# Performance work log

Hardware: AMD Instinct MI355X
Metric: run time of the kernel (lower is better)

## Reference

```python
import jax, jax.numpy as jnp
import numpy as np


def setup_inputs() -> dict:
    key = jax.random.key(0)
    k1, k2, k3, k4 = jax.random.split(key, 4)
    c = 256
    x = jax.random.normal(k1, (4, c, 64, 64), dtype=jnp.float32)
    # 1x1 conv weights act as channel-mixing matrices
    w_qkv = jax.random.normal(k2, (3 * c, c), dtype=jnp.float32) * (1.0 / np.sqrt(c))
    w_out = jax.random.normal(k3, (c, c), dtype=jnp.float32) * (1.0 / np.sqrt(c))
    b_out = jax.random.normal(k4, (c,), dtype=jnp.float32) * 0.01
    return {"x": x, "w_qkv": w_qkv, "w_out": w_out, "b_out": b_out}


def reference(x, w_qkv, w_out, b_out):
    b, c, h, w = x.shape
    heads = 4
    d = c // heads
    scale = d ** (-0.5)
    hw = h * w

    # 1x1 conv (no bias): [b,3c,h,w]
    qkv = jnp.einsum('oc,bchw->bohw', w_qkv, x)
    q, k, v = jnp.split(qkv, 3, axis=1)

    def to_seq(t):
        # [b,c,h,w] -> [b,heads,hw,d]
        return t.reshape(b, heads, d, hw).transpose(0, 1, 3, 2)

    q, k, v = to_seq(q), to_seq(k), to_seq(v)

    sim = jnp.einsum('bhid,bhjd->bhij', q, k) * scale
    attn = jax.nn.softmax(sim, axis=-1)
    out = jnp.einsum('bhij,bhjd->bhid', attn, v)

    # [b,heads,hw,d] -> [b,c,h,w]
    out = out.transpose(0, 1, 3, 2).reshape(b, c, h, w)

    # output 1x1 conv with bias, plus residual
    proj = jnp.einsum('oc,bchw->bohw', w_out, out) + b_out[None, :, None, None]
    return x + proj
```

## Files before the change

kernel.cpp:

```cpp
#include <hip/hip_runtime.h>


#define HW 4096
#define CIN 256
#define LOG2E_DIV8 0.18033688011112042f
#define SM_SHIFT 8.0f

typedef __attribute__((ext_vector_type(8))) short short8v;
typedef __attribute__((ext_vector_type(4))) short short4v;
typedef __attribute__((ext_vector_type(4))) float float4v;
typedef __attribute__((ext_vector_type(16))) float f32x16;
typedef __attribute__((ext_vector_type(4))) unsigned int uint4v;

typedef const __attribute__((address_space(1))) unsigned int* gptr_t;
typedef __attribute__((address_space(3))) unsigned int* lptr_t;

static __device__ __forceinline__ unsigned short f2bf(float f) {
    unsigned int u = __float_as_uint(f);
    u += 0x7fff + ((u >> 16) & 1);
    return (unsigned short)(u >> 16);
}
static __device__ __forceinline__ unsigned int pkbf(float a, float b) {
    unsigned int r;
    asm("v_cvt_pk_bf16_f32 %0, %1, %2" : "=v"(r) : "v"(a), "v"(b));
    return r;
}
static __device__ __forceinline__ void pl32swap(unsigned int& a, unsigned int& b) {
    asm volatile("v_permlane32_swap_b32 %0, %1" : "+v"(a), "+v"(b));
}

__global__ __launch_bounds__(256) void cast_all_k(
    const float* __restrict__ w_qkv, const float* __restrict__ w_out,
    const float* __restrict__ x,
    unsigned short* __restrict__ wqb, unsigned short* __restrict__ wob,
    unsigned short* __restrict__ xt)
{
    const int bi = blockIdx.x;
    const int t = threadIdx.x;
    __shared__ float tile[64][65];

    if (bi < 192) {
        const int idx = bi * 1024 + t * 4;
        const float s = (idx < 256 * 256) ? LOG2E_DIV8 : 1.0f;
        const float4 v = *(const float4*)&w_qkv[idx];
        uint2 pk;
        pk.x = pkbf(v.x * s, v.y * s);
        pk.y = pkbf(v.z * s, v.w * s);
        *(uint2*)&wqb[idx] = pk;
    } else if (bi < 256) {
        const int idx = (bi - 192) * 1024 + t * 4;
        const float4 v = *(const float4*)&w_out[idx];
        uint2 pk;
        pk.x = pkbf(v.x, v.y);
        pk.y = pkbf(v.z, v.w);
        *(uint2*)&wob[idx] = pk;
    } else {
        const int bx = bi - 256;
        const int p0 = (bx & 63) * 64;
        const int c0 = ((bx >> 6) & 3) * 64;
        const int b  = bx >> 8;

        const float* xb = x + ((size_t)b * CIN + c0) * HW + p0;
        #pragma unroll
        for (int iter = 0; iter < 4; ++iter) {
            const int idx = iter * 1024 + t * 4;
            const int cc = idx >> 6, pp = idx & 63;
            const float4 v = *(const float4*)&xb[(size_t)cc * HW + pp];
            tile[cc][pp + 0] = v.x; tile[cc][pp + 1] = v.y;
            tile[cc][pp + 2] = v.z; tile[cc][pp + 3] = v.w;
        }
        __syncthreads();
        unsigned short* xo = xt + ((size_t)b * HW + p0) * CIN + c0;
        #pragma unroll
        for (int iter = 0; iter < 4; ++iter) {
            const int idx = iter * 1024 + t * 4;
            const int pp = idx >> 6, cc = idx & 63;
            uint2 pk;
            pk.x = pkbf(tile[cc + 0][pp], tile[cc + 1][pp]);
            pk.y = pkbf(tile[cc + 2][pp], tile[cc + 3][pp]);
            *(uint2*)&xo[(size_t)pp * CIN + cc] = pk;
        }
    }
}

__global__ __launch_bounds__(256) void qkv_mfma_k(
    const unsigned short* __restrict__ wqb, const unsigned short* __restrict__ xt,
    unsigned short* __restrict__ qb, unsigned short* __restrict__ kb,
    unsigned short* __restrict__ vb)
{
    const int o0 = blockIdx.x * 128;
    const int p0 = blockIdx.y * 128;
    const int b  = blockIdx.z;
    const int t = threadIdx.x;
    const int wid = t >> 6, lane = t & 63, g = lane >> 4, li = lane & 15;
    const int wo = (wid >> 1) * 64, wp = (wid & 1) * 64;

    __shared__ char alds[16384];
    __shared__ char blds[16384];

    const int srow8 = t >> 3, sc16 = t & 7;
    const char* asrc = (const char*)wqb + ((size_t)(o0 + srow8) * 256) * 2 + sc16 * 16;
    const char* bsrc = (const char*)xt + (((size_t)b * HW + p0 + srow8) * 256) * 2 + sc16 * 16;

    float4 areg[4], breg[4];
    #pragma unroll
    for (int it = 0; it < 4; ++it) {
        areg[it] = *(const float4*)(asrc + (size_t)it * 32 * 512);
        breg[it] = *(const float4*)(bsrc + (size_t)it * 32 * 512);
    }

    float4v acc[4][4];
    #pragma unroll
    for (int mt = 0; mt < 4; ++mt)
        #pragma unroll
        for (int nt = 0; nt < 4; ++nt) acc[mt][nt] = (float4v){0.f, 0.f, 0.f, 0.f};

    for (int ks = 0; ks < 4; ++ks) {
        #pragma unroll
        for (int it = 0; it < 4; ++it) {
            const int row = it * 32 + srow8;
            const int dsw = row * 128 + ((sc16 * 16) ^ ((row & 7) << 4));
            *(float4*)(alds + dsw) = areg[it];
            *(float4*)(blds + dsw) = breg[it];
        }
        __syncthreads();
        if (ks < 3) {
            #pragma unroll
            for (int it = 0; it < 4; ++it) {
                areg[it] = *(const float4*)(asrc + (size_t)it * 32 * 512 + (ks + 1) * 128);
                breg[it] = *(const float4*)(bsrc + (size_t)it * 32 * 512 + (ks + 1) * 128);
            }
        }
        short8v af[4][2], bf[4][2];
        #pragma unroll
        for (int mt = 0; mt < 4; ++mt) {
            const int row = wo + mt * 16 + li;
            #pragma unroll
            for (int kc = 0; kc < 2; ++kc)
                af[mt][kc] = *(const short8v*)(alds + row * 128 + ((kc * 64 + g * 16) ^ ((row & 7) << 4)));
        }
        #pragma unroll
        for (int nt = 0; nt < 4; ++nt) {
            const int row = wp + nt * 16 + li;
            #pragma unroll
            for (int kc = 0; kc < 2; ++kc)
                bf[nt][kc] = *(const short8v*)(blds + row * 128 + ((kc * 64 + g * 16) ^ ((row & 7) << 4)));
        }
        #pragma unroll
        for (int mt = 0; mt < 4; ++mt)
            #pragma unroll
            for (int nt = 0; nt < 4; ++nt) {
                acc[mt][nt] = __builtin_amdgcn_mfma_f32_16x16x32_bf16(af[mt][0], bf[nt][0], acc[mt][nt], 0, 0, 0);
                acc[mt][nt] = __builtin_amdgcn_mfma_f32_16x16x32_bf16(af[mt][1], bf[nt][1], acc[mt][nt], 0, 0, 0);
            }
        __syncthreads();
    }

    const int which = o0 >> 8;
    #pragma unroll
    for (int mt = 0; mt < 4; ++mt) {
        const int o_b = o0 + wo + mt * 16 + g * 4;
        const int head = (o_b >> 6) & 3;
        const int dd = o_b & 63;
        const int bh = b * 4 + head;
        if (which < 2) {
            unsigned short* dst = which ? kb : qb;
            #pragma unroll
            for (int nt = 0; nt < 4; ++nt) {
                const int p = p0 + wp + nt * 16 + li;
                uint2 pk;
                pk.x = pkbf(acc[mt][nt][0], acc[mt][nt][1]);
                pk.y = pkbf(acc[mt][nt][2], acc[mt][nt][3]);
                *(uint2*)&dst[((size_t)bh * HW + p) * 64 + dd] = pk;
            }
        } else {
            #pragma unroll
            for (int nt = 0; nt < 4; ++nt) {
                const int p = p0 + wp + nt * 16 + li;
                #pragma unroll
                for (int r = 0; r < 4; ++r)
                    vb[((size_t)bh * 64 + dd + r) * HW + p] = f2bf(acc[mt][nt][r]);
            }
        }
    }
}

__global__ __launch_bounds__(512, 2) void flash_mfma_k(
    const unsigned short* __restrict__ qb, const unsigned short* __restrict__ kb,
    const unsigned short* __restrict__ vb, unsigned short* __restrict__ att)
{
    const int i0 = blockIdx.x * 128;
    const int bh = blockIdx.y;
    const int t = threadIdx.x;
    const int wid = t >> 6, lane = t & 63;
    const int q32 = lane & 31, hi = lane >> 5;
    const int sp = t >> 8;
    const int w4 = wid & 3;
    const int b = bh >> 2, head = bh & 3;

    const unsigned short* qg = qb + (size_t)bh * HW * 64;
    const unsigned short* kg = kb + (size_t)bh * HW * 64 + (size_t)sp * 2048 * 64;
    const unsigned short* vg = vb + (size_t)bh * 64 * HW + (size_t)sp * 2048;

    __shared__ char smem[65536];
    char* const kls = smem + sp * 16384;
    char* const vls = smem + 32768 + sp * 16384;

    const int q = i0 + w4 * 32 + q32;
    short8v qf[4];
    #pragma unroll
    for (int kc = 0; kc < 4; ++kc)
        qf[kc] = *(const short8v*)(qg + (size_t)q * 64 + kc * 16 + hi * 8);

    float l = 0.f;
    f32x16 acco[2];
    f32x16 accs[2];
    short8v pf[2][2];
    #pragma unroll
    for (int r = 0; r < 16; ++r) { acco[0][r] = 0.f; acco[1][r] = 0.f; }

    const int ts = t & 255;
    const int srow = ts >> 3;
    const int scol = (ts & 7) * 16;
    const int ssw  = (srow & 7) << 4;
    const char* kgsrc0 = (const char*)kg + (size_t)srow * 128 + (scol ^ ssw);
    const char* kgsrc1 = kgsrc0 + 32 * 128;
    const char* vgsrc0 = (const char*)vg + (size_t)srow * 8192 + (scol ^ ssw);
    const char* vgsrc1 = vgsrc0 + (size_t)32 * 8192;

    auto ISSUE = [&](int tile, int buf) {
        __builtin_amdgcn_global_load_lds(
            (gptr_t)(kgsrc0 + (size_t)tile * 8192),
            (lptr_t)(kls + buf * 8192 + ts * 16), 16, 0, 0);
        __builtin_amdgcn_global_load_lds(
            (gptr_t)(kgsrc1 + (size_t)tile * 8192),
            (lptr_t)(kls + buf * 8192 + 4096 + ts * 16), 16, 0, 0);
        __builtin_amdgcn_global_load_lds(
            (gptr_t)(vgsrc0 + (size_t)tile * 128),
            (lptr_t)(vls + buf * 8192 + ts * 16), 16, 0, 0);
        __builtin_amdgcn_global_load_lds(
            (gptr_t)(vgsrc1 + (size_t)tile * 128),
            (lptr_t)(vls + buf * 8192 + 4096 + ts * 16), 16, 0, 0);
    };
    auto SMM = [&](int buf) {
        #pragma unroll
        for (int r = 0; r < 16; ++r) { accs[0][r] = -SM_SHIFT; accs[1][r] = -SM_SHIFT; }
        __builtin_amdgcn_s_setprio(1);
        #pragma unroll
        for (int jt = 0; jt < 2; ++jt) {
            const int row = jt * 32 + q32;
            const char* kbase = kls + buf * 8192 + row * 128;
            const int sw = (row & 7) << 4;
            #pragma unroll
            for (int kc = 0; kc < 4; ++kc) {
                const short8v kf = *(const short8v*)(kbase + ((kc * 32 + hi * 16) ^ sw));
                accs[jt] = __builtin_amdgcn_mfma_f32_32x32x16_bf16(kf, qf[kc], accs[jt], 0, 0, 0);
            }
        }
        __builtin_amdgcn_s_setprio(0);
    };
    auto SOFT = [&]() {
        float ls = 0.f;
        #pragma unroll
        for (int jt = 0; jt < 2; ++jt) {
            float p[16];
            #pragma unroll
            for (int r = 0; r < 16; ++r) p[r] = __builtin_amdgcn_exp2f(accs[jt][r]);
            float s0 = (p[0] + p[1]) + (p[2] + p[3]);
            float s1 = (p[4] + p[5]) + (p[6] + p[7]);
            float s2 = (p[8] + p[9]) + (p[10] + p[11]);
            float s3 = (p[12] + p[13]) + (p[14] + p[15]);
            ls += (s0 + s1) + (s2 + s3);
            unsigned int w0 = pkbf(p[0], p[1]);
            unsigned int w1 = pkbf(p[2], p[3]);
            unsigned int w2 = pkbf(p[4], p[5]);
            unsigned int w3 = pkbf(p[6], p[7]);
            pl32swap(w0, w2);
            pl32swap(w1, w3);
            uint4v fa; fa[0] = w0; fa[1] = w1; fa[2] = w2; fa[3] = w3;
            pf[jt][0] = __builtin_bit_cast(short8v, fa);
            unsigned int w4_ = pkbf(p[8],  p[9]);
            unsigned int w5 = pkbf(p[10], p[11]);
            unsigned int w6 = pkbf(p[12], p[13]);
            unsigned int w7 = pkbf(p[14], p[15]);
            pl32swap(w4_, w6);
            pl32swap(w5, w7);
            uint4v fb; fb[0] = w4_; fb[1] = w5; fb[2] = w6; fb[3] = w7;
            pf[jt][1] = __builtin_bit_cast(short8v, fb);
        }
        l += ls;
    };
    auto PVMM = [&](int buf) {
        __builtin_amdgcn_s_setprio(1);
        #pragma unroll
        for (int dt = 0; dt < 2; ++dt) {
            const int row = dt * 32 + q32;
            const char* vbase = vls + buf * 8192 + row * 128;
            const int sw = (row & 7) << 4;
            #pragma unroll
            for (int jt = 0; jt < 2; ++jt)
                #pragma unroll
                for (int kr = 0; kr < 2; ++kr) {
                    const short8v vf = *(const short8v*)(vbase + ((jt * 64 + kr * 32 + hi * 16) ^ sw));
                    acco[dt] = __builtin_amdgcn_mfma_f32_32x32x16_bf16(vf, pf[jt][kr], acco[dt], 0, 0, 0);
                }
        }
        __builtin_amdgcn_s_setprio(0);
    };

    ISSUE(0, 0);
    __syncthreads();

    int buf = 0;
    for (int kt = 0; kt < 32; ++kt) {
        if (kt < 31) ISSUE(kt + 1, buf ^ 1);
        SMM(buf);
        SOFT();
        PVMM(buf);
        __syncthreads();
        buf ^= 1;
    }

    float* ex  = (float*)smem;
    float* lx  = (float*)(smem + 32768);
    const float ltot = l + __shfl_xor(l, 32, 64);
    if (sp == 1) {
        #pragma unroll
        for (int dt = 0; dt < 2; ++dt)
            #pragma unroll
            for (int r = 0; r < 16; ++r) {
                const int d = dt * 32 + 8 * (r >> 2) + 4 * hi + (r & 3);
                ex[w4 * 2048 + d * 32 + q32] = acco[dt][r];
            }
        if (hi == 0) lx[w4 * 32 + q32] = ltot;
    }
    __syncthreads();
    if (sp == 0) {
        const float inv = 1.0f / (ltot + lx[w4 * 32 + q32]);
        unsigned short* ao = att + ((size_t)b * HW + q) * CIN + head * 64;
        #pragma unroll
        for (int dt = 0; dt < 2; ++dt)
            #pragma unroll
            for (int g4 = 0; g4 < 4; ++g4) {
                const int d0 = dt * 32 + 8 * g4 + 4 * hi;
                const float* exb = ex + w4 * 2048 + d0 * 32 + q32;
                const float v0 = (acco[dt][g4 * 4 + 0] + exb[0])  * inv;
                const float v1 = (acco[dt][g4 * 4 + 1] + exb[32]) * inv;
                const float v2 = (acco[dt][g4 * 4 + 2] + exb[64]) * inv;
                const float v3 = (acco[dt][g4 * 4 + 3] + exb[96]) * inv;
                uint2 pk;
                pk.x = pkbf(v0, v1);
                pk.y = pkbf(v2, v3);
                *(uint2*)&ao[d0] = pk;
            }
    }
}

__global__ __launch_bounds__(256) void proj_mfma_k(
    const unsigned short* __restrict__ wob, const unsigned short* __restrict__ att,
    const float* __restrict__ bias, const float* __restrict__ x,
    float* __restrict__ out)
{
    const int o0 = blockIdx.x * 128;
    const int p0 = blockIdx.y * 128;
    const int b  = blockIdx.z;
    const int t = threadIdx.x;
    const int wid = t >> 6, lane = t & 63, g = lane >> 4, li = lane & 15;
    const int wo = (wid >> 1) * 64, wp = (wid & 1) * 64;

    __shared__ char alds[16384];
    __shared__ char blds[16384];

    const int srow8 = t >> 3, sc16 = t & 7;
    const char* asrc = (const char*)wob + ((size_t)(o0 + srow8) * 256) * 2 + sc16 * 16;
    const char* bsrc = (const char*)att + (((size_t)b * HW + p0 + srow8) * 256) * 2 + sc16 * 16;

    float4 areg[4], breg[4];
    #pragma unroll
    for (int it = 0; it < 4; ++it) {
        areg[it] = *(const float4*)(asrc + (size_t)it * 32 * 512);
        breg[it] = *(const float4*)(bsrc + (size_t)it * 32 * 512);
    }

    float4v acc[4][4];
    #pragma unroll
    for (int mt = 0; mt < 4; ++mt)
        #pragma unroll
        for (int nt = 0; nt < 4; ++nt) acc[mt][nt] = (float4v){0.f, 0.f, 0.f, 0.f};

    for (int ks = 0; ks < 4; ++ks) {
        #pragma unroll
        for (int it = 0; it < 4; ++it) {
            const int row = it * 32 + srow8;
            const int dsw = row * 128 + ((sc16 * 16) ^ ((row & 7) << 4));
            *(float4*)(alds + dsw) = areg[it];
            *(float4*)(blds + dsw) = breg[it];
        }
        __syncthreads();
        if (ks < 3) {
            #pragma unroll
            for (int it = 0; it < 4; ++it) {
                areg[it] = *(const float4*)(asrc + (size_t)it * 32 * 512 + (ks + 1) * 128);
                breg[it] = *(const float4*)(bsrc + (size_t)it * 32 * 512 + (ks + 1) * 128);
            }
        }
        short8v af[4][2], bf[4][2];
        #pragma unroll
        for (int mt = 0; mt < 4; ++mt) {
            const int row = wo + mt * 16 + li;
            #pragma unroll
            for (int kc = 0; kc < 2; ++kc)
                af[mt][kc] = *(const short8v*)(alds + row * 128 + ((kc * 64 + g * 16) ^ ((row & 7) << 4)));
        }
        #pragma unroll
        for (int nt = 0; nt < 4; ++nt) {
            const int row = wp + nt * 16 + li;
            #pragma unroll
            for (int kc = 0; kc < 2; ++kc)
                bf[nt][kc] = *(const short8v*)(blds + row * 128 + ((kc * 64 + g * 16) ^ ((row & 7) << 4)));
        }
        #pragma unroll
        for (int mt = 0; mt < 4; ++mt)
            #pragma unroll
            for (int nt = 0; nt < 4; ++nt) {
                acc[mt][nt] = __builtin_amdgcn_mfma_f32_16x16x32_bf16(af[mt][0], bf[nt][0], acc[mt][nt], 0, 0, 0);
                acc[mt][nt] = __builtin_amdgcn_mfma_f32_16x16x32_bf16(af[mt][1], bf[nt][1], acc[mt][nt], 0, 0, 0);
            }
        __syncthreads();
    }

    #pragma unroll
    for (int mt = 0; mt < 4; ++mt) {
        const int o_b = o0 + wo + mt * 16 + g * 4;
        #pragma unroll
        for (int nt = 0; nt < 4; ++nt) {
            const int p = p0 + wp + nt * 16 + li;
            #pragma unroll
            for (int r = 0; r < 4; ++r) {
                const int o = o_b + r;
                const size_t ix = ((size_t)b * CIN + o) * HW + p;
                out[ix] = acc[mt][nt][r] + bias[o] + x[ix];
            }
        }
    }
}

extern "C" void kernel_launch(void* const* d_in, const int* in_sizes, int n_in,
                              void* d_out, int out_size, void* d_ws, size_t ws_size,
                              hipStream_t stream)
{
    const float* x     = (const float*)d_in[0];
    const float* w_qkv = (const float*)d_in[1];
    const float* w_out = (const float*)d_in[2];
    const float* b_out = (const float*)d_in[3];
    float* out = (float*)d_out;

    char* ws = (char*)d_ws;
    const size_t MB = 1024 * 1024;
    unsigned short* xt  = (unsigned short*)(ws);
    unsigned short* qb  = (unsigned short*)(ws + 8 * MB);
    unsigned short* kb  = (unsigned short*)(ws + 16 * MB);
    unsigned short* vb  = (unsigned short*)(ws + 24 * MB);
    unsigned short* att = (unsigned short*)(ws + 32 * MB);
    unsigned short* wqb = (unsigned short*)(ws + 40 * MB);
    unsigned short* wob = (unsigned short*)(ws + 40 * MB + 768 * 256 * 2);

    cast_all_k<<<1280, 256, 0, stream>>>(w_qkv, w_out, x, wqb, wob, xt);
    qkv_mfma_k<<<dim3(6, 32, 4), 256, 0, stream>>>(wqb, xt, qb, kb, vb);
    flash_mfma_k<<<dim3(32, 16), 512, 0, stream>>>(qb, kb, vb, att);
    proj_mfma_k<<<dim3(2, 32, 4), 256, 0, stream>>>(wob, att, b_out, x, out);
}
```

Baseline: 140.0 us.

## Split flash attention KV halves into separate blocks with combine kernel

The key/value split moves from two halves inside one 512-thread block to separate 256-thread blocks along a third grid dimension. Each block writes its partial output as bf16 and its row sums to workspace, and a new combine kernel adds the two halves and normalizes. This removes the in-block shared-memory reduction and barrier and lets more smaller blocks be resident per CU. In exchange it adds an extra kernel launch, global round-trip traffic for the partials, and bf16 rounding of the partial sums before they are combined.

```diff
diff --git a/kernel.cpp b/kernel.cpp
--- a/kernel.cpp
+++ b/kernel.cpp
@@ -19,6 +19,9 @@
     unsigned int u = __float_as_uint(f);
     u += 0x7fff + ((u >> 16) & 1);
     return (unsigned short)(u >> 16);
+}
+static __device__ __forceinline__ float bf2f(unsigned short v) {
+    return __uint_as_float((unsigned int)v << 16);
 }
 static __device__ __forceinline__ unsigned int pkbf(float a, float b) {
     unsigned int r;
@@ -185,28 +188,26 @@
     }
 }
 
-__global__ __launch_bounds__(512, 2) void flash_mfma_k(
+__global__ __launch_bounds__(256, 4) void flash_mfma_k(
     const unsigned short* __restrict__ qb, const unsigned short* __restrict__ kb,
-    const unsigned short* __restrict__ vb, unsigned short* __restrict__ att)
+    const unsigned short* __restrict__ vb, unsigned short* __restrict__ po,
+    float* __restrict__ pl)
 {
     const int i0 = blockIdx.x * 128;
     const int bh = blockIdx.y;
+    const int sp = blockIdx.z;
     const int t = threadIdx.x;
     const int wid = t >> 6, lane = t & 63;
     const int q32 = lane & 31, hi = lane >> 5;
-    const int sp = t >> 8;
-    const int w4 = wid & 3;
-    const int b = bh >> 2, head = bh & 3;
 
     const unsigned short* qg = qb + (size_t)bh * HW * 64;
     const unsigned short* kg = kb + (size_t)bh * HW * 64 + (size_t)sp * 2048 * 64;
     const unsigned short* vg = vb + (size_t)bh * 64 * HW + (size_t)sp * 2048;
 
-    __shared__ char smem[65536];
-    char* const kls = smem + sp * 16384;
-    char* const vls = smem + 32768 + sp * 16384;
-
-    const int q = i0 + w4 * 32 + q32;
+    __shared__ char klds[2][8192];
+    __shared__ char vlds[2][8192];
+
+    const int q = i0 + wid * 32 + q32;
     short8v qf[4];
     #pragma unroll
     for (int kc = 0; kc < 4; ++kc)
@@ -219,9 +220,8 @@
     #pragma unroll
     for (int r = 0; r < 16; ++r) { acco[0][r] = 0.f; acco[1][r] = 0.f; }
 
-    const int ts = t & 255;
-    const int srow = ts >> 3;
-    const int scol = (ts & 7) * 16;
+    const int srow = t >> 3;
+    const int scol = (t & 7) * 16;
     const int ssw  = (srow & 7) << 4;
     const char* kgsrc0 = (const char*)kg + (size_t)srow * 128 + (scol ^ ssw);
     const char* kgsrc1 = kgsrc0 + 32 * 128;
@@ -231,16 +231,16 @@
     auto ISSUE = [&](int tile, int buf) {
         __builtin_amdgcn_global_load_lds(
             (gptr_t)(kgsrc0 + (size_t)tile * 8192),
-            (lptr_t)(kls + buf * 8192 + ts * 16), 16, 0, 0);
+            (lptr_t)(klds[buf] + t * 16), 16, 0, 0);
         __builtin_amdgcn_global_load_lds(
             (gptr_t)(kgsrc1 + (size_t)tile * 8192),
-            (lptr_t)(kls + buf * 8192 + 4096 + ts * 16), 16, 0, 0);
+            (lptr_t)(klds[buf] + 4096 + t * 16), 16, 0, 0);
         __builtin_amdgcn_global_load_lds(
             (gptr_t)(vgsrc0 + (size_t)tile * 128),
-            (lptr_t)(vls + buf * 8192 + ts * 16), 16, 0, 0);
+            (lptr_t)(vlds[buf] + t * 16), 16, 0, 0);
         __builtin_amdgcn_global_load_lds(
             (gptr_t)(vgsrc1 + (size_t)tile * 128),
-            (lptr_t)(vls + buf * 8192 + 4096 + ts * 16), 16, 0, 0);
+            (lptr_t)(vlds[buf] + 4096 + t * 16), 16, 0, 0);
     };
     auto SMM = [&](int buf) {
         #pragma unroll
@@ -249,7 +249,7 @@
         #pragma unroll
         for (int jt = 0; jt < 2; ++jt) {
             const int row = jt * 32 + q32;
-            const char* kbase = kls + buf * 8192 + row * 128;
+            const char* kbase = klds[buf] + row * 128;
             const int sw = (row & 7) << 4;
             #pragma unroll
             for (int kc = 0; kc < 4; ++kc) {
@@ -295,7 +295,7 @@
         #pragma unroll
         for (int dt = 0; dt < 2; ++dt) {
             const int row = dt * 32 + q32;
-            const char* vbase = vls + buf * 8192 + row * 128;
+            const char* vbase = vlds[buf] + row * 128;
             const int sw = (row & 7) << 4;
             #pragma unroll
             for (int jt = 0; jt < 2; ++jt)
@@ -321,38 +321,51 @@
         buf ^= 1;
     }
 
-    float* ex  = (float*)smem;
-    float* lx  = (float*)(smem + 32768);
     const float ltot = l + __shfl_xor(l, 32, 64);
-    if (sp == 1) {
-        #pragma unroll
-        for (int dt = 0; dt < 2; ++dt)
-            #pragma unroll
-            for (int r = 0; r < 16; ++r) {
-                const int d = dt * 32 + 8 * (r >> 2) + 4 * hi + (r & 3);
-                ex[w4 * 2048 + d * 32 + q32] = acco[dt][r];
-            }
-        if (hi == 0) lx[w4 * 32 + q32] = ltot;
-    }
-    __syncthreads();
-    if (sp == 0) {
-        const float inv = 1.0f / (ltot + lx[w4 * 32 + q32]);
-        unsigned short* ao = att + ((size_t)b * HW + q) * CIN + head * 64;
-        #pragma unroll
-        for (int dt = 0; dt < 2; ++dt)
-            #pragma unroll
-            for (int g4 = 0; g4 < 4; ++g4) {
-                const int d0 = dt * 32 + 8 * g4 + 4 * hi;
-                const float* exb = ex + w4 * 2048 + d0 * 32 + q32;
-                const float v0 = (acco[dt][g4 * 4 + 0] + exb[0])  * inv;
-                const float v1 = (acco[dt][g4 * 4 + 1] + exb[32]) * inv;
-                const float v2 = (acco[dt][g4 * 4 + 2] + exb[64]) * inv;
-                const float v3 = (acco[dt][g4 * 4 + 3] + exb[96]) * inv;
-                uint2 pk;
-                pk.x = pkbf(v0, v1);
-                pk.y = pkbf(v2, v3);
-                *(uint2*)&ao[d0] = pk;
-            }
+    unsigned short* prow = po + ((size_t)(sp * 16 + bh) * HW + q) * 64;
+    #pragma unroll
+    for (int dt = 0; dt < 2; ++dt)
+        #pragma unroll
+        for (int g4 = 0; g4 < 4; ++g4) {
+            const int d0 = dt * 32 + 8 * g4 + 4 * hi;
+            uint2 pk;
+            pk.x = pkbf(acco[dt][g4 * 4 + 0], acco[dt][g4 * 4 + 1]);
+            pk.y = pkbf(acco[dt][g4 * 4 + 2], acco[dt][g4 * 4 + 3]);
+            *(uint2*)&prow[d0] = pk;
+        }
+    if (hi == 0) pl[(size_t)(sp * 16 + bh) * HW + q] = ltot;
+}
+
+__global__ __launch_bounds__(256) void combine_k(
+    const unsigned short* __restrict__ po, const float* __restrict__ pl,
+    unsigned short* __restrict__ att)
+{
+    const int gid = blockIdx.x * 256 + threadIdx.x;
+    const int half = gid & 1;
+    const int q = (gid >> 1) & 4095;
+    const int bh = gid >> 13;
+    const int b = bh >> 2, head = bh & 3;
+
+    const size_t r0 = (size_t)bh * HW + q;
+    const size_t r1 = (size_t)(16 + bh) * HW + q;
+    const float inv = 1.0f / (pl[r0] + pl[r1]);
+
+    const unsigned short* p0 = po + r0 * 64 + half * 32;
+    const unsigned short* p1 = po + r1 * 64 + half * 32;
+    unsigned short* ao = att + ((size_t)b * HW + q) * CIN + head * 64 + half * 32;
+
+    #pragma unroll
+    for (int w = 0; w < 4; ++w) {
+        const short8v a = *(const short8v*)(p0 + w * 8);
+        const short8v c = *(const short8v*)(p1 + w * 8);
+        uint4v r;
+        #pragma unroll
+        for (int i = 0; i < 4; ++i) {
+            const float lo = (bf2f((unsigned short)a[2 * i])     + bf2f((unsigned short)c[2 * i]))     * inv;
+            const float hv = (bf2f((unsigned short)a[2 * i + 1]) + bf2f((unsigned short)c[2 * i + 1])) * inv;
+            r[i] = pkbf(lo, hv);
+        }
+        *(uint4v*)(ao + w * 8) = r;
     }
 }
 
@@ -464,9 +477,12 @@
     unsigned short* att = (unsigned short*)(ws + 32 * MB);
     unsigned short* wqb = (unsigned short*)(ws + 40 * MB);
     unsigned short* wob = (unsigned short*)(ws + 40 * MB + 768 * 256 * 2);
+    unsigned short* po  = (unsigned short*)(ws + 41 * MB);
+    float*          pl  = (float*)(ws + 57 * MB);
 
     cast_all_k<<<1280, 256, 0, stream>>>(w_qkv, w_out, x, wqb, wob, xt);
     qkv_mfma_k<<<dim3(6, 32, 4), 256, 0, stream>>>(wqb, xt, qb, kb, vb);
-    flash_mfma_k<<<dim3(32, 16), 512, 0, stream>>>(qb, kb, vb, att);
+    flash_mfma_k<<<dim3(32, 16, 2), 256, 0, stream>>>(qb, kb, vb, po, pl);
+    combine_k<<<512, 256, 0, stream>>>(po, pl, att);
     proj_mfma_k<<<dim3(2, 32, 4), 256, 0, stream>>>(wob, att, b_out, x, out);
 }
```

After: 144.6 us. 1.03x slower.
